# Kernel optimization log

Hardware: AMD Instinct MI355X
Metric: run time of the kernel (lower is better)

## Reference

```python
import jax, jax.numpy as jnp
import numpy as np

B, S, H, F, E, K = 4, 2048, 1024, 3584, 8, 2


def setup_inputs() -> dict:
    key = jax.random.key(0)
    ks = jax.random.split(key, 5)
    sc = 0.02
    return {
        "hidden_states": jax.random.normal(ks[0], (B, S, H), jnp.float32),
        "router_w": jax.random.normal(ks[1], (E, H), jnp.float32) * sc,
        "w1": jax.random.normal(ks[2], (E, F, H), jnp.float32) * sc,
        "v1": jax.random.normal(ks[3], (E, F, H), jnp.float32) * sc,
        "w2": jax.random.normal(ks[4], (E, F, H), jnp.float32) * sc,
    }


def reference(hidden_states, router_w, w1, v1, w2):
    b, s, h = hidden_states.shape
    x = hidden_states.reshape(-1, h)  # [T, H] tokens (transpose(0,1) is a no-op per-token)
    T = x.shape[0]
    n_exp = w1.shape[0]

    # --- Mixtral router: fp32 softmax, top-k, renormalize ---
    logits = x @ router_w.T  # [T, E]
    scores = jax.nn.softmax(logits.astype(jnp.float32), axis=-1)
    expert_weights, expert_indices = jax.lax.top_k(scores, K)  # [T, K]
    expert_weights = expert_weights / expert_weights.sum(axis=-1, keepdims=True)
    expert_weights = expert_weights.astype(x.dtype)

    # combine coefficients: coef[t, e] = sum_k weight[t,k] * (idx[t,k]==e)
    coef = jnp.zeros((T, n_exp), x.dtype)
    coef = coef.at[jnp.arange(T)[:, None], expert_indices].add(expert_weights)

    out = jnp.zeros_like(x)
    for e in range(n_exp):  # small fixed expert count
        hmid = jax.nn.silu(x @ w1[e].T) * (x @ v1[e].T)  # [T, F]
        out = out + coef[:, e:e + 1] * (hmid @ w2[e])  # [T, H]
    return out.reshape(b, s, h)
```

## Files before the change

### kernel.cpp

```cpp
#include <hip/hip_runtime.h>
#include <cstdint>
#include <cstddef>

#define T_TOK 8192
#define H_DIM 1024
#define F_DIM 3584
#define E_NUM 8
#define MAX_ROWS 17408
#define MAX_TILES 136

typedef __bf16 bf16_t;
typedef bf16_t bf16x8 __attribute__((ext_vector_type(8)));
typedef bf16_t bf16x4 __attribute__((ext_vector_type(4)));
typedef float floatx4 __attribute__((ext_vector_type(4)));

typedef const __attribute__((address_space(1))) void* gas_ptr;
typedef __attribute__((address_space(3))) void* las_ptr;

__device__ __forceinline__ void async_copy16(const void* g, void* l) {
    __builtin_amdgcn_global_load_lds((gas_ptr)g, (las_ptr)l, 16, 0, 0);
}

__global__ void cast_f32_to_bf16(const float* __restrict__ in, bf16_t* __restrict__ out, int n4) {
    int i = blockIdx.x * blockDim.x + threadIdx.x;
    if (i < n4) {
        const float4 v = ((const float4*)in)[i];
        bf16x4 o;
        o[0] = (bf16_t)v.x; o[1] = (bf16_t)v.y; o[2] = (bf16_t)v.z; o[3] = (bf16_t)v.w;
        ((bf16x4*)out)[i] = o;
    }
}

__global__ void transpose_cast_w2(const float* __restrict__ W2, bf16_t* __restrict__ W2T) {
    __shared__ bf16_t tile[32][34];
    const int e = blockIdx.z;
    const int f0 = blockIdx.x * 32;
    const int h0 = blockIdx.y * 32;
    const float* src = W2 + (size_t)e * F_DIM * H_DIM;
    bf16_t* dst = W2T + (size_t)e * H_DIM * F_DIM;
    const int tx = threadIdx.x;
    const int ty = threadIdx.y;
#pragma unroll
    for (int r = 0; r < 32; r += 8)
        tile[ty + r][tx] = (bf16_t)src[(size_t)(f0 + ty + r) * H_DIM + (h0 + tx)];
    __syncthreads();
#pragma unroll
    for (int r = 0; r < 32; r += 8)
        dst[(size_t)(h0 + ty + r) * F_DIM + (f0 + tx)] = tile[tx][ty + r];
}

__global__ void router_kernel(const float* __restrict__ X, const float* __restrict__ RW,
                              int* __restrict__ tok_e, float* __restrict__ tok_w) {
    const int lane = threadIdx.x & 63;
    const int wave = threadIdx.x >> 6;
    const int t = blockIdx.x * 4 + wave;
    const float* xp = X + (size_t)t * H_DIM;
    float xr[16];
#pragma unroll
    for (int j = 0; j < 16; ++j) xr[j] = xp[j * 64 + lane];
    float logits[E_NUM];
#pragma unroll
    for (int e = 0; e < E_NUM; ++e) {
        const float* rp = RW + e * H_DIM;
        float a = 0.f;
#pragma unroll
        for (int j = 0; j < 16; ++j) a += xr[j] * rp[j * 64 + lane];
#pragma unroll
        for (int s = 32; s; s >>= 1) a += __shfl_xor(a, s, 64);
        logits[e] = a;
    }
    if (lane == 0) {
        float mx = logits[0];
#pragma unroll
        for (int e = 1; e < E_NUM; ++e) mx = fmaxf(mx, logits[e]);
        float p[E_NUM], sum = 0.f;
#pragma unroll
        for (int e = 0; e < E_NUM; ++e) { p[e] = __expf(logits[e] - mx); sum += p[e]; }
#pragma unroll
        for (int e = 0; e < E_NUM; ++e) p[e] /= sum;
        int i0 = 0;
#pragma unroll
        for (int e = 1; e < E_NUM; ++e) if (p[e] > p[i0]) i0 = e;
        int i1 = (i0 == 0) ? 1 : 0;
#pragma unroll
        for (int e = 0; e < E_NUM; ++e) if (e != i0 && p[e] > p[i1]) i1 = e;
        const float s2 = p[i0] + p[i1];
        tok_e[t * 2 + 0] = i0; tok_w[t * 2 + 0] = p[i0] / s2;
        tok_e[t * 2 + 1] = i1; tok_w[t * 2 + 1] = p[i1] / s2;
    }
}

__global__ void build_assignments(const int* __restrict__ tok_e, const float* __restrict__ tok_w,
                                  int* __restrict__ asg_tok, float* __restrict__ asg_wt,
                                  int* __restrict__ tok_slot, int* __restrict__ tile_meta,
                                  int* __restrict__ n_tiles_out) {
    __shared__ int cnt[E_NUM];
    __shared__ int seg_start[E_NUM];
    __shared__ int seg_pad[E_NUM];
    const int tid = threadIdx.x;
    if (tid < E_NUM) cnt[tid] = 0;
    __syncthreads();
    for (int i = tid; i < T_TOK * 2; i += 1024) atomicAdd(&cnt[tok_e[i]], 1);
    __syncthreads();
    if (tid == 0) {
        int run = 0, nt = 0;
        for (int e = 0; e < E_NUM; ++e) {
            seg_start[e] = run;
            const int tiles = (cnt[e] + 127) >> 7;
            seg_pad[e] = tiles << 7;
            for (int j = 0; j < tiles; ++j) {
                tile_meta[nt * 2] = e;
                tile_meta[nt * 2 + 1] = run + j * 128;
                ++nt;
            }
            run += tiles << 7;
        }
        *n_tiles_out = nt;
    }
    __syncthreads();
    if (tid < E_NUM) cnt[tid] = 0;
    __syncthreads();
    for (int i = tid; i < T_TOK * 2; i += 1024) {
        const int e = tok_e[i];
        const int slot = atomicAdd(&cnt[e], 1);
        const int g = seg_start[e] + slot;
        asg_tok[g] = i >> 1;
        asg_wt[g] = tok_w[i];
        tok_slot[i] = g;
    }
    __syncthreads();
    for (int e = 0; e < E_NUM; ++e)
        for (int j = cnt[e] + tid; j < seg_pad[e]; j += 1024) {
            asg_tok[seg_start[e] + j] = -1;
            asg_wt[seg_start[e] + j] = 0.f;
        }
}


__global__ __launch_bounds__(256, 2)
void gemm1_glu(const bf16_t* __restrict__ X, const bf16_t* __restrict__ W1all,
               const bf16_t* __restrict__ V1all, const int* __restrict__ asg_tok,
               const float* __restrict__ asg_wt, const int* __restrict__ tile_meta,
               const int* __restrict__ n_tiles, bf16_t* __restrict__ Hmid) {
    const int tile = blockIdx.x;
    if (tile >= *n_tiles) return;
    const int e = tile_meta[tile * 2];
    const int row0 = tile_meta[tile * 2 + 1];
    const bf16_t* W1 = W1all + (size_t)e * F_DIM * H_DIM;
    const bf16_t* V1 = V1all + (size_t)e * F_DIM * H_DIM;

    __shared__ __attribute__((aligned(16))) bf16_t As[128 * 32];
    __shared__ __attribute__((aligned(16))) bf16_t B1s[128 * 32];
    __shared__ __attribute__((aligned(16))) bf16_t B2s[128 * 32];
    const int tid = threadIdx.x;
    const int lane = tid & 63;
    const int wave = tid >> 6;
    const int n0 = blockIdx.y * 128;
    const int wm = (wave >> 1) * 64;
    const int wn = (wave & 1) * 64;
    const int fr = lane & 15;
    const int q = lane >> 4;

    floatx4 acc1[4][4], acc2[4][4];
    const floatx4 zero = {0.f, 0.f, 0.f, 0.f};
#pragma unroll
    for (int a = 0; a < 4; ++a)
#pragma unroll
        for (int b = 0; b < 4; ++b) { acc1[a][b] = zero; acc2[a][b] = zero; }

    const int srow = tid >> 2;
    const int c = ((tid & 3) - ((tid >> 3) & 3)) & 3;
    const int scc = c * 8;
    const int ldsb0 = (tid & 192) * 16;
    const int ldsb1 = 4096 + ldsb0;

    int t0 = asg_tok[row0 + srow];      if (t0 < 0) t0 = 0;
    int t1 = asg_tok[row0 + 64 + srow]; if (t1 < 0) t1 = 0;
    const bf16_t* a0p = X + (size_t)t0 * H_DIM + scc;
    const bf16_t* a1p = X + (size_t)t1 * H_DIM + scc;
    const bf16_t* b1p0 = W1 + (size_t)(n0 + srow) * H_DIM + scc;
    const bf16_t* b1p1 = W1 + (size_t)(n0 + 64 + srow) * H_DIM + scc;
    const bf16_t* b2p0 = V1 + (size_t)(n0 + srow) * H_DIM + scc;
    const bf16_t* b2p1 = V1 + (size_t)(n0 + 64 + srow) * H_DIM + scc;

    for (int k0 = 0; k0 < H_DIM; k0 += 32) {
        async_copy16(a0p + k0, (char*)As + ldsb0);
        async_copy16(a1p + k0, (char*)As + ldsb1);
        async_copy16(b1p0 + k0, (char*)B1s + ldsb0);
        async_copy16(b1p1 + k0, (char*)B1s + ldsb1);
        async_copy16(b2p0 + k0, (char*)B2s + ldsb0);
        async_copy16(b2p1 + k0, (char*)B2s + ldsb1);
        __syncthreads();

        bf16x8 af[4], b1f[4], b2f[4];
#pragma unroll
        for (int mi = 0; mi < 4; ++mi) {
            const int r = wm + mi * 16 + fr;
            const int sl = (q + ((r >> 1) & 3)) & 3;
            af[mi] = *(const bf16x8*)&As[r * 32 + sl * 8];
        }
#pragma unroll
        for (int ni = 0; ni < 4; ++ni) {
            const int r = wn + ni * 16 + fr;
            const int sl = (q + ((r >> 1) & 3)) & 3;
            b1f[ni] = *(const bf16x8*)&B1s[r * 32 + sl * 8];
            b2f[ni] = *(const bf16x8*)&B2s[r * 32 + sl * 8];
        }
#pragma unroll
        for (int mi = 0; mi < 4; ++mi)
#pragma unroll
            for (int ni = 0; ni < 4; ++ni) {
                acc1[mi][ni] = __builtin_amdgcn_mfma_f32_16x16x32_bf16(af[mi], b1f[ni], acc1[mi][ni], 0, 0, 0);
                acc2[mi][ni] = __builtin_amdgcn_mfma_f32_16x16x32_bf16(af[mi], b2f[ni], acc2[mi][ni], 0, 0, 0);
            }
        __syncthreads();
    }

#pragma unroll
    for (int mi = 0; mi < 4; ++mi) {
#pragma unroll
        for (int r = 0; r < 4; ++r) {
            const int gr = row0 + wm + mi * 16 + q * 4 + r;
            const float wt = asg_wt[gr];
            bf16_t* hp = Hmid + (size_t)gr * F_DIM + n0 + wn + fr;
#pragma unroll
            for (int ni = 0; ni < 4; ++ni) {
                const float s1 = acc1[mi][ni][r];
                const float s2 = acc2[mi][ni][r];
                const float val = (s1 / (1.f + __expf(-s1))) * s2 * wt;
                hp[ni * 16] = (bf16_t)val;
            }
        }
    }
}

__global__ __launch_bounds__(256, 2)
void gemm2_out(const bf16_t* __restrict__ Hmid, const bf16_t* __restrict__ W2Tall,
               const int* __restrict__ tile_meta, const int* __restrict__ n_tiles,
               float* __restrict__ Oasm) {
    const int tile = blockIdx.x;
    if (tile >= *n_tiles) return;
    const int e = tile_meta[tile * 2];
    const int row0 = tile_meta[tile * 2 + 1];
    const bf16_t* W2T = W2Tall + (size_t)e * H_DIM * F_DIM;

    __shared__ __attribute__((aligned(16))) bf16_t As[128 * 32];
    __shared__ __attribute__((aligned(16))) bf16_t Bs[128 * 32];
    const int tid = threadIdx.x;
    const int lane = tid & 63;
    const int wave = tid >> 6;
    const int n0 = blockIdx.y * 128;
    const int wm = (wave >> 1) * 64;
    const int wn = (wave & 1) * 64;
    const int fr = lane & 15;
    const int q = lane >> 4;

    floatx4 acc[4][4];
    const floatx4 zero = {0.f, 0.f, 0.f, 0.f};
#pragma unroll
    for (int a = 0; a < 4; ++a)
#pragma unroll
        for (int b = 0; b < 4; ++b) acc[a][b] = zero;

    const int srow = tid >> 2;
    const int c = ((tid & 3) - ((tid >> 3) & 3)) & 3;
    const int scc = c * 8;
    const int ldsb0 = (tid & 192) * 16;
    const int ldsb1 = 4096 + ldsb0;

    const bf16_t* a0p = Hmid + (size_t)(row0 + srow) * F_DIM + scc;
    const bf16_t* a1p = Hmid + (size_t)(row0 + 64 + srow) * F_DIM + scc;
    const bf16_t* b0p = W2T + (size_t)(n0 + srow) * F_DIM + scc;
    const bf16_t* b1p = W2T + (size_t)(n0 + 64 + srow) * F_DIM + scc;

    for (int k0 = 0; k0 < F_DIM; k0 += 32) {
        async_copy16(a0p + k0, (char*)As + ldsb0);
        async_copy16(a1p + k0, (char*)As + ldsb1);
        async_copy16(b0p + k0, (char*)Bs + ldsb0);
        async_copy16(b1p + k0, (char*)Bs + ldsb1);
        __syncthreads();

        bf16x8 af[4], bf[4];
#pragma unroll
        for (int mi = 0; mi < 4; ++mi) {
            const int r = wm + mi * 16 + fr;
            const int sl = (q + ((r >> 1) & 3)) & 3;
            af[mi] = *(const bf16x8*)&As[r * 32 + sl * 8];
        }
#pragma unroll
        for (int ni = 0; ni < 4; ++ni) {
            const int r = wn + ni * 16 + fr;
            const int sl = (q + ((r >> 1) & 3)) & 3;
            bf[ni] = *(const bf16x8*)&Bs[r * 32 + sl * 8];
        }
#pragma unroll
        for (int mi = 0; mi < 4; ++mi)
#pragma unroll
            for (int ni = 0; ni < 4; ++ni)
                acc[mi][ni] = __builtin_amdgcn_mfma_f32_16x16x32_bf16(af[mi], bf[ni], acc[mi][ni], 0, 0, 0);
        __syncthreads();
    }

#pragma unroll
    for (int mi = 0; mi < 4; ++mi) {
#pragma unroll
        for (int r = 0; r < 4; ++r) {
            const int gr = row0 + wm + mi * 16 + q * 4 + r;
            float* op = Oasm + (size_t)gr * H_DIM + n0 + wn + fr;
#pragma unroll
            for (int ni = 0; ni < 4; ++ni)
                op[ni * 16] = acc[mi][ni][r];
        }
    }
}

__global__ void combine_kernel(const float* __restrict__ Oasm, const int* __restrict__ tok_slot,
                               float* __restrict__ Out) {
    const int t = blockIdx.x;
    const int s0 = tok_slot[t * 2];
    const int s1 = tok_slot[t * 2 + 1];
    const float4 v0 = ((const float4*)(Oasm + (size_t)s0 * H_DIM))[threadIdx.x];
    const float4 v1 = ((const float4*)(Oasm + (size_t)s1 * H_DIM))[threadIdx.x];
    float4 o; o.x = v0.x + v1.x; o.y = v0.y + v1.y; o.z = v0.z + v1.z; o.w = v0.w + v1.w;
    ((float4*)(Out + (size_t)t * H_DIM))[threadIdx.x] = o;
}

extern "C" void kernel_launch(void* const* d_in, const int* in_sizes, int n_in,
                              void* d_out, int out_size, void* d_ws, size_t ws_size,
                              hipStream_t stream) {
    const float* x  = (const float*)d_in[0];
    const float* rw = (const float*)d_in[1];
    const float* w1 = (const float*)d_in[2];
    const float* v1 = (const float*)d_in[3];
    const float* w2 = (const float*)d_in[4];
    float* out = (float*)d_out;

    char* ws = (char*)d_ws;
    const size_t MB = 1024 * 1024;
    bf16_t* xb   = (bf16_t*)(ws + 0);
    bf16_t* w1b  = (bf16_t*)(ws + 16 * MB);
    bf16_t* v1b  = (bf16_t*)(ws + 72 * MB);
    bf16_t* hmid = (bf16_t*)(ws + 128 * MB);
    bf16_t* w2t  = (bf16_t*)(ws + 0);
    float*  oasm = (float*)(ws + 56 * MB);
    char* meta = ws + 128 * MB + (size_t)MAX_ROWS * F_DIM * 2;
    int*   asg_tok  = (int*)meta;                meta += MAX_ROWS * 4;
    float* asg_wt   = (float*)meta;              meta += MAX_ROWS * 4;
    int*   tok_slot = (int*)meta;                meta += T_TOK * 2 * 4;
    int*   tok_e    = (int*)meta;                meta += T_TOK * 2 * 4;
    float* tok_w    = (float*)meta;              meta += T_TOK * 2 * 4;
    int*   tile_meta = (int*)meta;               meta += MAX_TILES * 2 * 4;
    int*   n_tiles   = (int*)meta;               meta += 4;

    const int nx4 = T_TOK * H_DIM / 4;
    const int nw4 = E_NUM * F_DIM * H_DIM / 4;
    cast_f32_to_bf16<<<nx4 / 256, 256, 0, stream>>>(x, xb, nx4);
    cast_f32_to_bf16<<<nw4 / 256, 256, 0, stream>>>(w1, w1b, nw4);
    cast_f32_to_bf16<<<nw4 / 256, 256, 0, stream>>>(v1, v1b, nw4);
    router_kernel<<<T_TOK / 4, 256, 0, stream>>>(x, rw, tok_e, tok_w);
    build_assignments<<<1, 1024, 0, stream>>>(tok_e, tok_w, asg_tok, asg_wt,
                                              tok_slot, tile_meta, n_tiles);
    gemm1_glu<<<dim3(MAX_TILES, F_DIM / 128), 256, 0, stream>>>(
        xb, w1b, v1b, asg_tok, asg_wt, tile_meta, n_tiles, hmid);
    transpose_cast_w2<<<dim3(F_DIM / 32, H_DIM / 32, E_NUM), dim3(32, 8), 0, stream>>>(w2, w2t);
    gemm2_out<<<dim3(MAX_TILES, H_DIM / 128), 256, 0, stream>>>(
        hmid, w2t, tile_meta, n_tiles, oasm);
    combine_kernel<<<T_TOK, 256, 0, stream>>>(oasm, tok_slot, out);
}
```

Baseline: 926.0 us.

## Double-buffer LDS tiles and remap block order in both MoE GEMMs

Both expert GEMM kernels now use two LDS buffers, issuing the async global-to-LDS loads for the next K slice before computing on the current one. Each iteration ends with a vmcnt wait and a barrier, and the MFMA section runs at raised wave priority. This aims to hide global load latency behind matrix math. Block indices are also remapped so consecutive launches spread across tiles and N-blocks, changing cache locality of the shared weights. LDS use doubles, which may limit the two-blocks-per-CU occupancy, and a single barrier per iteration leaves the buffer-reuse safety dependent on the vmcnt wait.

```diff
diff --git a/kernel.cpp b/kernel.cpp
--- a/kernel.cpp
+++ b/kernel.cpp
@@ -20,6 +20,9 @@
 __device__ __forceinline__ void async_copy16(const void* g, void* l) {
     __builtin_amdgcn_global_load_lds((gas_ptr)g, (las_ptr)l, 16, 0, 0);
 }
+
+#define WAIT_VM0() asm volatile("s_waitcnt vmcnt(0)" ::: "memory")
+#define BAR() __builtin_amdgcn_s_barrier()
 
 __global__ void cast_f32_to_bf16(const float* __restrict__ in, bf16_t* __restrict__ out, int n4) {
     int i = blockIdx.x * blockDim.x + threadIdx.x;
@@ -142,20 +145,23 @@
                const bf16_t* __restrict__ V1all, const int* __restrict__ asg_tok,
                const float* __restrict__ asg_wt, const int* __restrict__ tile_meta,
                const int* __restrict__ n_tiles, bf16_t* __restrict__ Hmid) {
-    const int tile = blockIdx.x;
+    const int lin = blockIdx.x + MAX_TILES * blockIdx.y;
+    const int w = (lin & 7) * (MAX_TILES * 28 / 8) + (lin >> 3);
+    const int tile = w % MAX_TILES;
+    const int nb = w / MAX_TILES;
     if (tile >= *n_tiles) return;
     const int e = tile_meta[tile * 2];
     const int row0 = tile_meta[tile * 2 + 1];
     const bf16_t* W1 = W1all + (size_t)e * F_DIM * H_DIM;
     const bf16_t* V1 = V1all + (size_t)e * F_DIM * H_DIM;
 
-    __shared__ __attribute__((aligned(16))) bf16_t As[128 * 32];
-    __shared__ __attribute__((aligned(16))) bf16_t B1s[128 * 32];
-    __shared__ __attribute__((aligned(16))) bf16_t B2s[128 * 32];
+    __shared__ __attribute__((aligned(16))) bf16_t As[2][128 * 32];
+    __shared__ __attribute__((aligned(16))) bf16_t B1s[2][128 * 32];
+    __shared__ __attribute__((aligned(16))) bf16_t B2s[2][128 * 32];
     const int tid = threadIdx.x;
     const int lane = tid & 63;
     const int wave = tid >> 6;
-    const int n0 = blockIdx.y * 128;
+    const int n0 = nb * 128;
     const int wm = (wave >> 1) * 64;
     const int wn = (wave & 1) * 64;
     const int fr = lane & 15;
@@ -183,29 +189,48 @@
     const bf16_t* b2p0 = V1 + (size_t)(n0 + srow) * H_DIM + scc;
     const bf16_t* b2p1 = V1 + (size_t)(n0 + 64 + srow) * H_DIM + scc;
 
-    for (int k0 = 0; k0 < H_DIM; k0 += 32) {
-        async_copy16(a0p + k0, (char*)As + ldsb0);
-        async_copy16(a1p + k0, (char*)As + ldsb1);
-        async_copy16(b1p0 + k0, (char*)B1s + ldsb0);
-        async_copy16(b1p1 + k0, (char*)B1s + ldsb1);
-        async_copy16(b2p0 + k0, (char*)B2s + ldsb0);
-        async_copy16(b2p1 + k0, (char*)B2s + ldsb1);
-        __syncthreads();
-
+    const int NT = H_DIM / 32;
+
+    async_copy16(a0p,  (char*)As[0]  + ldsb0);
+    async_copy16(a1p,  (char*)As[0]  + ldsb1);
+    async_copy16(b1p0, (char*)B1s[0] + ldsb0);
+    async_copy16(b1p1, (char*)B1s[0] + ldsb1);
+    async_copy16(b2p0, (char*)B2s[0] + ldsb0);
+    async_copy16(b2p1, (char*)B2s[0] + ldsb1);
+    WAIT_VM0();
+    BAR();
+
+    for (int t = 0; t < NT; ++t) {
+        const int cur = t & 1;
+        if (t + 1 < NT) {
+            const int k = (t + 1) * 32;
+            async_copy16(a0p + k,  (char*)As[cur ^ 1]  + ldsb0);
+            async_copy16(a1p + k,  (char*)As[cur ^ 1]  + ldsb1);
+            async_copy16(b1p0 + k, (char*)B1s[cur ^ 1] + ldsb0);
+            async_copy16(b1p1 + k, (char*)B1s[cur ^ 1] + ldsb1);
+            async_copy16(b2p0 + k, (char*)B2s[cur ^ 1] + ldsb0);
+            async_copy16(b2p1 + k, (char*)B2s[cur ^ 1] + ldsb1);
+        }
+        __builtin_amdgcn_sched_barrier(0);
+
+        const bf16_t* Ar  = As[cur];
+        const bf16_t* B1r = B1s[cur];
+        const bf16_t* B2r = B2s[cur];
         bf16x8 af[4], b1f[4], b2f[4];
 #pragma unroll
         for (int mi = 0; mi < 4; ++mi) {
             const int r = wm + mi * 16 + fr;
             const int sl = (q + ((r >> 1) & 3)) & 3;
-            af[mi] = *(const bf16x8*)&As[r * 32 + sl * 8];
+            af[mi] = *(const bf16x8*)&Ar[r * 32 + sl * 8];
         }
 #pragma unroll
         for (int ni = 0; ni < 4; ++ni) {
             const int r = wn + ni * 16 + fr;
             const int sl = (q + ((r >> 1) & 3)) & 3;
-            b1f[ni] = *(const bf16x8*)&B1s[r * 32 + sl * 8];
-            b2f[ni] = *(const bf16x8*)&B2s[r * 32 + sl * 8];
-        }
+            b1f[ni] = *(const bf16x8*)&B1r[r * 32 + sl * 8];
+            b2f[ni] = *(const bf16x8*)&B2r[r * 32 + sl * 8];
+        }
+        __builtin_amdgcn_s_setprio(1);
 #pragma unroll
         for (int mi = 0; mi < 4; ++mi)
 #pragma unroll
@@ -213,7 +238,11 @@
                 acc1[mi][ni] = __builtin_amdgcn_mfma_f32_16x16x32_bf16(af[mi], b1f[ni], acc1[mi][ni], 0, 0, 0);
                 acc2[mi][ni] = __builtin_amdgcn_mfma_f32_16x16x32_bf16(af[mi], b2f[ni], acc2[mi][ni], 0, 0, 0);
             }
-        __syncthreads();
+        __builtin_amdgcn_s_setprio(0);
+        if (t + 1 < NT) {
+            WAIT_VM0();
+            BAR();
+        }
     }
 
 #pragma unroll
@@ -238,18 +267,20 @@
 void gemm2_out(const bf16_t* __restrict__ Hmid, const bf16_t* __restrict__ W2Tall,
                const int* __restrict__ tile_meta, const int* __restrict__ n_tiles,
                float* __restrict__ Oasm) {
-    const int tile = blockIdx.x;
+    const int lin = blockIdx.x + MAX_TILES * blockIdx.y;
+    const int w = (lin & 7) * MAX_TILES + (lin >> 3);
+    const int tile = w >> 3;
+    const int n0 = (w & 7) * 128;
     if (tile >= *n_tiles) return;
     const int e = tile_meta[tile * 2];
     const int row0 = tile_meta[tile * 2 + 1];
     const bf16_t* W2T = W2Tall + (size_t)e * H_DIM * F_DIM;
 
-    __shared__ __attribute__((aligned(16))) bf16_t As[128 * 32];
-    __shared__ __attribute__((aligned(16))) bf16_t Bs[128 * 32];
+    __shared__ __attribute__((aligned(16))) bf16_t As[2][128 * 32];
+    __shared__ __attribute__((aligned(16))) bf16_t Bs[2][128 * 32];
     const int tid = threadIdx.x;
     const int lane = tid & 63;
     const int wave = tid >> 6;
-    const int n0 = blockIdx.y * 128;
     const int wm = (wave >> 1) * 64;
     const int wn = (wave & 1) * 64;
     const int fr = lane & 15;
@@ -273,32 +304,52 @@
     const bf16_t* b0p = W2T + (size_t)(n0 + srow) * F_DIM + scc;
     const bf16_t* b1p = W2T + (size_t)(n0 + 64 + srow) * F_DIM + scc;
 
-    for (int k0 = 0; k0 < F_DIM; k0 += 32) {
-        async_copy16(a0p + k0, (char*)As + ldsb0);
-        async_copy16(a1p + k0, (char*)As + ldsb1);
-        async_copy16(b0p + k0, (char*)Bs + ldsb0);
-        async_copy16(b1p + k0, (char*)Bs + ldsb1);
-        __syncthreads();
-
+    const int NT = F_DIM / 32;
+
+    async_copy16(a0p, (char*)As[0] + ldsb0);
+    async_copy16(a1p, (char*)As[0] + ldsb1);
+    async_copy16(b0p, (char*)Bs[0] + ldsb0);
+    async_copy16(b1p, (char*)Bs[0] + ldsb1);
+    WAIT_VM0();
+    BAR();
+
+    for (int t = 0; t < NT; ++t) {
+        const int cur = t & 1;
+        if (t + 1 < NT) {
+            const int k = (t + 1) * 32;
+            async_copy16(a0p + k, (char*)As[cur ^ 1] + ldsb0);
+            async_copy16(a1p + k, (char*)As[cur ^ 1] + ldsb1);
+            async_copy16(b0p + k, (char*)Bs[cur ^ 1] + ldsb0);
+            async_copy16(b1p + k, (char*)Bs[cur ^ 1] + ldsb1);
+        }
+        __builtin_amdgcn_sched_barrier(0);
+
+        const bf16_t* Ar = As[cur];
+        const bf16_t* Br = Bs[cur];
         bf16x8 af[4], bf[4];
 #pragma unroll
         for (int mi = 0; mi < 4; ++mi) {
             const int r = wm + mi * 16 + fr;
             const int sl = (q + ((r >> 1) & 3)) & 3;
-            af[mi] = *(const bf16x8*)&As[r * 32 + sl * 8];
+            af[mi] = *(const bf16x8*)&Ar[r * 32 + sl * 8];
         }
 #pragma unroll
         for (int ni = 0; ni < 4; ++ni) {
             const int r = wn + ni * 16 + fr;
             const int sl = (q + ((r >> 1) & 3)) & 3;
-            bf[ni] = *(const bf16x8*)&Bs[r * 32 + sl * 8];
-        }
+            bf[ni] = *(const bf16x8*)&Br[r * 32 + sl * 8];
+        }
+        __builtin_amdgcn_s_setprio(1);
 #pragma unroll
         for (int mi = 0; mi < 4; ++mi)
 #pragma unroll
             for (int ni = 0; ni < 4; ++ni)
                 acc[mi][ni] = __builtin_amdgcn_mfma_f32_16x16x32_bf16(af[mi], bf[ni], acc[mi][ni], 0, 0, 0);
-        __syncthreads();
+        __builtin_amdgcn_s_setprio(0);
+        if (t + 1 < NT) {
+            WAIT_VM0();
+            BAR();
+        }
     }
 
 #pragma unroll
```

Measured after the change: 921.9 us. No clear change (-0.4%).
